# Optimization experiments

Measured on AMD Instinct MI355X. Metric: run time of the kernel, lower is better.

## Reference

```python
import jax, jax.numpy as jnp
import numpy as np

NUM_HEADS = 16
D_MODEL = 1024
DEPTH = D_MODEL // NUM_HEADS
THRESHOLD = 0.1
BATCH = 2
SEQ = 2048


def setup_inputs() -> dict:
    key = jax.random.key(0)
    ks = jax.random.split(key, 9)
    w_scale = 1.0 / np.sqrt(D_MODEL)
    Q = jax.random.normal(ks[0], (BATCH, SEQ, D_MODEL), dtype=jnp.float32)
    T = jax.random.normal(ks[1], (BATCH, SEQ, D_MODEL), dtype=jnp.float32)
    V = jax.random.normal(ks[2], (BATCH, SEQ, D_MODEL), dtype=jnp.float32)
    Wq = jax.random.normal(ks[3], (NUM_HEADS, D_MODEL, DEPTH), dtype=jnp.float32) * w_scale
    Wk = jax.random.normal(ks[4], (NUM_HEADS, D_MODEL, DEPTH), dtype=jnp.float32) * w_scale
    Wv = jax.random.normal(ks[5], (NUM_HEADS, D_MODEL, DEPTH), dtype=jnp.float32) * w_scale
    Wo = jax.random.normal(ks[6], (D_MODEL, D_MODEL), dtype=jnp.float32) * w_scale
    bq = jnp.zeros((NUM_HEADS, DEPTH), dtype=jnp.float32)
    bk = jnp.zeros((NUM_HEADS, DEPTH), dtype=jnp.float32)
    bv = jnp.zeros((NUM_HEADS, DEPTH), dtype=jnp.float32)
    bo = jnp.zeros((D_MODEL,), dtype=jnp.float32)
    return {"Q": Q, "T": T, "V": V, "Wq": Wq, "bq": bq, "Wk": Wk, "bk": bk,
            "Wv": Wv, "bv": bv, "Wo": Wo, "bo": bo}


def reference(Q, T, V, Wq, bq, Wk, bk, Wv, bv, Wo, bo):
    # Per-head projections (stacked over heads): [B,S,D] x [H,D,E] -> [B,H,S,E]
    q = jnp.einsum('bsd,hde->bhse', Q, Wq) + bq[None, :, None, :]
    k = jnp.einsum('bsd,hde->bhse', T, Wk) + bk[None, :, None, :]
    v = jnp.einsum('bsd,hde->bhse', V, Wv) + bv[None, :, None, :]

    # Raw scores (NOT pre-scaled): [B,H,S,S]
    scores = jnp.einsum('bhqe,bhke->bhqk', q, k)
    # tf.where(A>thr, A, -2**32 * cast(A>thr)) -> failing entries become 0
    scores = jnp.where(scores > THRESHOLD, scores, jnp.zeros((), scores.dtype))
    # M = 1 - lower_band(ones): +1 on strictly upper-triangular entries
    seq = scores.shape[-1]
    upper = jnp.triu(jnp.ones((seq, seq), dtype=scores.dtype), k=1)
    scores = (scores + upper) / jnp.sqrt(jnp.asarray(DEPTH, scores.dtype))

    attn = jax.nn.softmax(scores, axis=-1)
    out = jnp.einsum('bhqk,bhke->bhqe', attn, v)  # [B,H,S,E]
    B, H, S, E = out.shape
    concat = out.transpose(0, 2, 1, 3).reshape(B, S, H * E)  # [B,S,D]
    return concat @ Wo + bo
```

## Files before the change

### kernel.cpp

```cpp
#include <hip/hip_runtime.h>
#include <stdint.h>


typedef __attribute__((ext_vector_type(8))) short bf16x8;
typedef __attribute__((ext_vector_type(4))) float f32x4;

#define DEVFN static __device__ __forceinline__

static constexpr int S_ = 2048;
static constexpr int H_ = 16;

DEVFN unsigned short f2bf(float x) {
  union { float f; uint32_t u; } v; v.f = x;
  const uint32_t r = v.u + 0x7fffu + ((v.u >> 16) & 1u);
  return (unsigned short)(r >> 16);
}

DEVFN f32x4 fzero() { f32x4 v = {0.f, 0.f, 0.f, 0.f}; return v; }

union U8 { uint32_t u[4]; bf16x8 v; };

DEVFN void gld_lds16(const void* g, void* lds) {
  __builtin_amdgcn_global_load_lds(
      (const __attribute__((address_space(1))) void*)g,
      (__attribute__((address_space(3))) void*)lds, 16, 0, 0);
}

__global__ void prep_weights(const float* __restrict__ Wq, const float* __restrict__ Wk,
                             const float* __restrict__ Wv, const float* __restrict__ Wo,
                             unsigned short* __restrict__ dstBase) {
  const int z = blockIdx.z;
  const float* src = (z == 0) ? Wq : (z == 1) ? Wk : (z == 2) ? Wv : Wo;
  unsigned short* dst = dstBase + (size_t)z * (1024u * 1024u);
  const int idx = blockIdx.x * 256 + threadIdx.x;
  const int c = idx & 1023;
  const int d0 = (idx >> 10) << 3;
  unsigned short hv[8];
#pragma unroll
  for (int t = 0; t < 8; ++t) {
    const int d = d0 + t;
    const float v = (z < 3) ? src[(size_t)((c >> 6) * 1024 + d) * 64 + (c & 63)]
                            : src[(size_t)d * 1024 + c];
    hv[t] = f2bf(v);
  }
  *(uint4*)(dst + (size_t)c * 1024 + d0) = *(const uint4*)hv;
}

__global__ __launch_bounds__(256, 3)
void proj_gemm(const float* __restrict__ Qm, const float* __restrict__ Tm,
               const float* __restrict__ Vm, const unsigned short* __restrict__ Wt,
               const float* __restrict__ bq, const float* __restrict__ bk,
               const float* __restrict__ bv, unsigned short* __restrict__ qb,
               unsigned short* __restrict__ kb, unsigned short* __restrict__ vtb) {
  __shared__ float Af[2][128 * 32];
  __shared__ unsigned short Bt[2][128 * 32];

  const int tid = threadIdx.x;
  const int lane = tid & 63;
  const int w = tid >> 6;
  const int g = lane >> 4, c = lane & 15;
  const int wm = w >> 1, wn = w & 1;

  const int m0 = blockIdx.x * 128;
  const int proj = blockIdx.y >> 3;
  const int n0 = (blockIdx.y & 7) * 128;

  const float* Asrc = (proj == 0) ? Qm : (proj == 1) ? Tm : Vm;
  const unsigned short* W = Wt + (size_t)proj * (1024u * 1024u);

  f32x4 acc[4][4];
#pragma unroll
  for (int i = 0; i < 4; ++i)
#pragma unroll
    for (int j = 0; j < 4; ++j) acc[i][j] = fzero();

  const int arow = w * 8 + (lane >> 3);
  const int ach = lane & 7;
  const int brow = w * 16 + (lane >> 2);
  const int bch = lane & 3;

  auto stage = [&](int kt, int buf) {
#pragma unroll
    for (int u = 0; u < 4; ++u) {
      const int row = u * 32 + arow;
      const int ch = ach ^ (row & 7);
      gld_lds16(Asrc + (size_t)(m0 + row) * 1024 + kt * 32 + ch * 4,
                &Af[buf][(u * 32 + w * 8) * 32]);
    }
#pragma unroll
    for (int u = 0; u < 2; ++u) {
      const int row = u * 64 + brow;
      const int ch = bch ^ ((row >> 1) & 3);
      gld_lds16(W + (size_t)(n0 + row) * 1024 + kt * 32 + ch * 8,
                &Bt[buf][(u * 64 + w * 16) * 32]);
    }
  };

  stage(0, 0);
  __syncthreads();

  for (int kt = 0; kt < 32; ++kt) {
    const int buf = kt & 1;
    if (kt < 31) stage(kt + 1, buf ^ 1);

    bf16x8 af[4], bfr[4];
#pragma unroll
    for (int mi = 0; mi < 4; ++mi) {
      const int row = wm * 64 + mi * 16 + c;
      const int swz = row & 7;
      const float4 fa = *(const float4*)&Af[buf][row * 32 + ((2 * g) ^ swz) * 4];
      const float4 fb = *(const float4*)&Af[buf][row * 32 + ((2 * g + 1) ^ swz) * 4];
      U8 u8;
      asm("v_cvt_pk_bf16_f32 %0, %1, %2" : "=v"(u8.u[0]) : "v"(fa.x), "v"(fa.y));
      asm("v_cvt_pk_bf16_f32 %0, %1, %2" : "=v"(u8.u[1]) : "v"(fa.z), "v"(fa.w));
      asm("v_cvt_pk_bf16_f32 %0, %1, %2" : "=v"(u8.u[2]) : "v"(fb.x), "v"(fb.y));
      asm("v_cvt_pk_bf16_f32 %0, %1, %2" : "=v"(u8.u[3]) : "v"(fb.z), "v"(fb.w));
      af[mi] = u8.v;
    }
#pragma unroll
    for (int ni = 0; ni < 4; ++ni) {
      const int row = wn * 64 + ni * 16 + c;
      bfr[ni] = *(const bf16x8*)&Bt[buf][row * 32 + ((g ^ ((row >> 1) & 3))) * 8];
    }
#pragma unroll
    for (int mi = 0; mi < 4; ++mi)
#pragma unroll
      for (int ni = 0; ni < 4; ++ni)
        acc[mi][ni] = __builtin_amdgcn_mfma_f32_16x16x32_bf16(af[mi], bfr[ni],
                                                              acc[mi][ni], 0, 0, 0);
    __syncthreads();
  }

  const float* bias = (proj == 0) ? bq : (proj == 1) ? bk : bv;
  if (proj < 2) {
    unsigned short* dptr = (proj == 0) ? qb : kb;
#pragma unroll
    for (int ni = 0; ni < 4; ++ni) {
      const int colb = n0 + wn * 64 + ni * 16 + c;
      const float bc = bias[colb];
      const int hh = colb >> 6, e = colb & 63;
#pragma unroll
      for (int mi = 0; mi < 4; ++mi)
#pragma unroll
        for (int r = 0; r < 4; ++r) {
          const int row = m0 + wm * 64 + mi * 16 + g * 4 + r;
          const int bb = row >> 11, s = row & 2047;
          dptr[(((size_t)(bb * H_ + hh)) * S_ + s) * 64 + e] = f2bf(acc[mi][ni][r] + bc);
        }
    }
  } else {
#pragma unroll
    for (int ni = 0; ni < 4; ++ni) {
      const int colb = n0 + wn * 64 + ni * 16 + c;
      const float bc = bias[colb];
      const int hh = colb >> 6, e = colb & 63;
#pragma unroll
      for (int mi = 0; mi < 4; ++mi) {
        const int rowb = m0 + wm * 64 + mi * 16 + g * 4;
        const int bb = rowb >> 11, s0 = rowb & 2047;
        const float v0 = acc[mi][ni][0] + bc, v1 = acc[mi][ni][1] + bc;
        const float v2 = acc[mi][ni][2] + bc, v3 = acc[mi][ni][3] + bc;
        uint2 pk;
        asm("v_cvt_pk_bf16_f32 %0, %1, %2" : "=v"(pk.x) : "v"(v0), "v"(v1));
        asm("v_cvt_pk_bf16_f32 %0, %1, %2" : "=v"(pk.y) : "v"(v2), "v"(v3));
        *(uint2*)&vtb[(((size_t)(bb * H_ + hh)) * 64 + e) * S_ + s0] = pk;
      }
    }
  }
}

__global__ __launch_bounds__(256, 2)
void attn_kernel(const unsigned short* __restrict__ qb,
                 const unsigned short* __restrict__ kb,
                 const unsigned short* __restrict__ vtb,
                 unsigned short* __restrict__ att) {
  __shared__ unsigned short Kt[2][64 * 64];
  __shared__ unsigned short Vt[2][64 * 64];
  __shared__ unsigned short Pt[4][32 * 64];

  const int tid = threadIdx.x;
  const int lane = tid & 63;
  const int w = tid >> 6;
  const int g = lane >> 4, c = lane & 15;

  const int orig = blockIdx.x;
  const int logical = ((orig & 7) << 6) | (orig >> 3);
  const int qblk = logical & 15;
  const int bh = logical >> 4;
  const int hh = bh & 15, bz = bh >> 4;

  const int q0w = qblk * 128 + w * 32;
  const unsigned short* qh = qb + (size_t)bh * S_ * 64;
  const unsigned short* kh = kb + (size_t)bh * S_ * 64;
  const unsigned short* vh = vtb + (size_t)bh * 64 * S_;

  bf16x8 aq[2][2];
#pragma unroll
  for (int m = 0; m < 2; ++m)
#pragma unroll
    for (int t = 0; t < 2; ++t)
      aq[m][t] = *(const bf16x8*)&qh[(size_t)(q0w + m * 16 + c) * 64 + t * 32 + g * 8];

  bf16x8 onesB;
#pragma unroll
  for (int i = 0; i < 8; ++i) onesB[i] = (short)0x3F80;

  f32x4 O[2][4];
  f32x4 accL[2];
#pragma unroll
  for (int m = 0; m < 2; ++m) {
#pragma unroll
    for (int ne = 0; ne < 4; ++ne) O[m][ne] = fzero();
    accL[m] = fzero();
  }

  constexpr float L2E = 1.4426950408889634f;
  const float S2 = 0.125f * L2E;
  const float B2 = 0.125f * L2E;

  int kvOff[2][4], paOff[2][2], pwOff[2][4];
#pragma unroll
  for (int ks = 0; ks < 2; ++ks) {
#pragma unroll
    for (int mi = 0; mi < 4; ++mi) {
      const int row = mi * 16 + c;
      kvOff[ks][mi] = 2 * (row * 64 + ((ks * 4 + g) ^ (row & 7)) * 8);
    }
#pragma unroll
    for (int m = 0; m < 2; ++m)
      paOff[m][ks] = 2 * ((m * 16 + c) * 64 + ((ks * 4 + g) ^ (c & 7)) * 8);
  }
#pragma unroll
  for (int m = 0; m < 2; ++m)
#pragma unroll
    for (int mi = 0; mi < 4; ++mi)
      pwOff[m][mi] =
          2 * ((m * 16 + c) * 64 + ((2 * mi + (g >> 1)) ^ (c & 7)) * 8 + (g & 1) * 4);

  const int srow = w * 8 + (lane >> 3);
  const int sch = (lane & 7) ^ (srow & 7);
  const unsigned short* kS0 = kh + (size_t)srow * 64 + sch * 8;
  const unsigned short* kS1 = kh + (size_t)(32 + srow) * 64 + sch * 8;
  const unsigned short* vS0 = vh + (size_t)srow * S_ + sch * 8;
  const unsigned short* vS1 = vh + (size_t)(32 + srow) * S_ + sch * 8;

  {
    gld_lds16(kS0, &Kt[0][(w * 8) * 64]);
    gld_lds16(kS1, &Kt[0][(32 + w * 8) * 64]);
    gld_lds16(vS0, &Vt[0][(w * 8) * 64]);
    gld_lds16(vS1, &Vt[0][(32 + w * 8) * 64]);
  }
  __syncthreads();

#define SM_ELEM(M, MI)                                                         \
  do {                                                                         \
    float pv[4];                                                               \
    if (allUp || noneUp) {                                                     \
      const float bb = allUp ? B2 : 0.f;                                       \
      _Pragma("unroll")                                                        \
      for (int r = 0; r < 4; ++r) {                                            \
        const float v = sa[M][MI][r];                                          \
        pv[r] = __builtin_amdgcn_exp2f(                                        \
            (v > 0.1f) ? __builtin_fmaf(v, S2, bb) : bb);                      \
      }                                                                        \
    } else {                                                                   \
      const int iq = q0w + (M)*16 + c;                                         \
      _Pragma("unroll")                                                        \
      for (int r = 0; r < 4; ++r) {                                            \
        const float v = sa[M][MI][r];                                          \
        const float bb = (j0 + (MI)*16 + g * 4 + r > iq) ? B2 : 0.f;           \
        pv[r] = __builtin_amdgcn_exp2f(                                        \
            (v > 0.1f) ? __builtin_fmaf(v, S2, bb) : bb);                      \
      }                                                                        \
    }                                                                          \
    uint2 d;                                                                   \
    asm("v_cvt_pk_bf16_f32 %0, %1, %2" : "=v"(d.x) : "v"(pv[0]), "v"(pv[1])); \
    asm("v_cvt_pk_bf16_f32 %0, %1, %2" : "=v"(d.y) : "v"(pv[2]), "v"(pv[3])); \
    *(uint2*)((char*)&Pt[w][0] + pwOff[M][MI]) = d;                            \
  } while (0)

#define PV_HALF(KS, CUR)                                                       \
  do {                                                                         \
    const bf16x8 pa0 =                                                         \
        *(const bf16x8*)((const char*)&Pt[w][0] + paOff[0][KS]);               \
    const bf16x8 pa1 =                                                         \
        *(const bf16x8*)((const char*)&Pt[w][0] + paOff[1][KS]);               \
    accL[0] = __builtin_amdgcn_mfma_f32_16x16x32_bf16(pa0, onesB, accL[0],     \
                                                      0, 0, 0);                \
    accL[1] = __builtin_amdgcn_mfma_f32_16x16x32_bf16(pa1, onesB, accL[1],     \
                                                      0, 0, 0);                \
    _Pragma("unroll")                                                          \
    for (int ne = 0; ne < 4; ++ne) {                                           \
      const bf16x8 bv8 =                                                       \
          *(const bf16x8*)((const char*)&Vt[CUR][0] + kvOff[KS][ne]);          \
      O[0][ne] = __builtin_amdgcn_mfma_f32_16x16x32_bf16(pa0, bv8, O[0][ne],   \
                                                         0, 0, 0);             \
      O[1][ne] = __builtin_amdgcn_mfma_f32_16x16x32_bf16(pa1, bv8, O[1][ne],   \
                                                         0, 0, 0);             \
    }                                                                          \
  } while (0)

#define ATTN_BODY(JT, CUR)                                                     \
  do {                                                                         \
    const int j0 = (JT) * 64;                                                  \
    if ((JT) < 31) {             \
      gld_lds16(kS0 + 4096, &Kt[CUR ^ 1][(w * 8) * 64]);                       \
      gld_lds16(kS1 + 4096, &Kt[CUR ^ 1][(32 + w * 8) * 64]);                  \
      gld_lds16(vS0 + 64, &Vt[CUR ^ 1][(w * 8) * 64]);                         \
      gld_lds16(vS1 + 64, &Vt[CUR ^ 1][(32 + w * 8) * 64]);                    \
      kS0 += 4096; kS1 += 4096; vS0 += 64; vS1 += 64;                          \
    }                                                                          \
    f32x4 sa[2][4];                                                            \
    _Pragma("unroll")                                                          \
    for (int m = 0; m < 2; ++m)                                                \
      _Pragma("unroll")                                                        \
      for (int mi = 0; mi < 4; ++mi) sa[m][mi] = fzero();                      \
    __builtin_amdgcn_s_setprio(1);                                             \
    _Pragma("unroll")                                                          \
    for (int ks = 0; ks < 2; ++ks)                                             \
      _Pragma("unroll")                                                        \
      for (int mi = 0; mi < 4; ++mi) {                                         \
        const bf16x8 ka =                                                      \
            *(const bf16x8*)((const char*)&Kt[CUR][0] + kvOff[ks][mi]);        \
        sa[0][mi] = __builtin_amdgcn_mfma_f32_16x16x32_bf16(ka, aq[0][ks],     \
                                                            sa[0][mi], 0, 0, 0);\
        sa[1][mi] = __builtin_amdgcn_mfma_f32_16x16x32_bf16(ka, aq[1][ks],     \
                                                            sa[1][mi], 0, 0, 0);\
      }                                                                        \
    __builtin_amdgcn_s_setprio(0);                                             \
    const bool allUp = (j0 >= q0w + 32);                                       \
    const bool noneUp = (j0 + 63 <= q0w);                                      \
              \
    SM_ELEM(0, 0); SM_ELEM(0, 1); SM_ELEM(1, 0); SM_ELEM(1, 1);                \
    asm volatile("s_waitcnt lgkmcnt(0)" ::: "memory");                         \
    __builtin_amdgcn_sched_barrier(0);                                         \
    __builtin_amdgcn_s_setprio(1);                                             \
    PV_HALF(0, CUR);             \
    __builtin_amdgcn_s_setprio(0);                                             \
                                           \
    SM_ELEM(0, 2); SM_ELEM(0, 3); SM_ELEM(1, 2); SM_ELEM(1, 3);                \
    asm volatile("s_waitcnt lgkmcnt(0)" ::: "memory");                         \
    __builtin_amdgcn_sched_barrier(0);                                         \
    __builtin_amdgcn_s_setprio(1);                                             \
    PV_HALF(1, CUR);                                                           \
    __builtin_amdgcn_s_setprio(0);                                             \
    __syncthreads();     \
  } while (0)

  for (int jt = 0; jt < 32; jt += 2) {
    ATTN_BODY(jt, 0);
    ATTN_BODY(jt + 1, 1);
  }
#undef ATTN_BODY
#undef PV_HALF
#undef SM_ELEM

#pragma unroll
  for (int m = 0; m < 2; ++m)
#pragma unroll
    for (int r = 0; r < 4; ++r) {
      const float il = 1.f / accL[m][r];
      const int qg = q0w + m * 16 + g * 4 + r;
      const size_t ro = ((size_t)(bz * S_ + qg)) * 1024 + hh * 64;
#pragma unroll
      for (int ne = 0; ne < 4; ++ne)
        att[ro + ne * 16 + c] = f2bf(O[m][ne][r] * il);
    }
}

__global__ __launch_bounds__(256, 3)
void out_gemm(const unsigned short* __restrict__ att,
              const unsigned short* __restrict__ WoT,
              const float* __restrict__ bo, float* __restrict__ outp) {
  __shared__ unsigned short At[2][128 * 32];
  __shared__ unsigned short Bt[2][128 * 32];

  const int tid = threadIdx.x;
  const int lane = tid & 63;
  const int w = tid >> 6;
  const int g = lane >> 4, c = lane & 15;
  const int wm = w >> 1, wn = w & 1;
  const int m0 = blockIdx.x * 128;
  const int n0 = blockIdx.y * 128;

  f32x4 acc[4][4];
#pragma unroll
  for (int i = 0; i < 4; ++i)
#pragma unroll
    for (int j = 0; j < 4; ++j) acc[i][j] = fzero();

  const int srow = lane >> 2;
  const int sch = lane & 3;

  auto stage = [&](int kt, int buf) {
#pragma unroll
    for (int u = 0; u < 2; ++u) {
      const int row = u * 64 + w * 16 + srow;
      const int ch = sch ^ ((row >> 1) & 3);
      gld_lds16(att + (size_t)(m0 + row) * 1024 + kt * 32 + ch * 8,
                &At[buf][(u * 64 + w * 16) * 32]);
      gld_lds16(WoT + (size_t)(n0 + row) * 1024 + kt * 32 + ch * 8,
                &Bt[buf][(u * 64 + w * 16) * 32]);
    }
  };

  stage(0, 0);
  __syncthreads();

  for (int kt = 0; kt < 32; ++kt) {
    const int buf = kt & 1;
    if (kt < 31) stage(kt + 1, buf ^ 1);

    bf16x8 af[4], bfr[4];
#pragma unroll
    for (int mi = 0; mi < 4; ++mi) {
      const int row = wm * 64 + mi * 16 + c;
      af[mi] = *(const bf16x8*)&At[buf][row * 32 + ((g ^ ((row >> 1) & 3))) * 8];
    }
#pragma unroll
    for (int ni = 0; ni < 4; ++ni) {
      const int row = wn * 64 + ni * 16 + c;
      bfr[ni] = *(const bf16x8*)&Bt[buf][row * 32 + ((g ^ ((row >> 1) & 3))) * 8];
    }
#pragma unroll
    for (int mi = 0; mi < 4; ++mi)
#pragma unroll
      for (int ni = 0; ni < 4; ++ni)
        acc[mi][ni] = __builtin_amdgcn_mfma_f32_16x16x32_bf16(af[mi], bfr[ni],
                                                              acc[mi][ni], 0, 0, 0);
    __syncthreads();
  }

#pragma unroll
  for (int ni = 0; ni < 4; ++ni) {
    const int colb = n0 + wn * 64 + ni * 16 + c;
    const float bc = bo[colb];
#pragma unroll
    for (int mi = 0; mi < 4; ++mi)
#pragma unroll
      for (int r = 0; r < 4; ++r) {
        const int row = m0 + wm * 64 + mi * 16 + g * 4 + r;
        outp[(size_t)row * 1024 + colb] = acc[mi][ni][r] + bc;
      }
  }
}

extern "C" void kernel_launch(void* const* d_in, const int* in_sizes, int n_in,
                              void* d_out, int out_size, void* d_ws, size_t ws_size,
                              hipStream_t stream) {
  const float* Q  = (const float*)d_in[0];
  const float* T  = (const float*)d_in[1];
  const float* V  = (const float*)d_in[2];
  const float* Wq = (const float*)d_in[3];
  const float* bq = (const float*)d_in[4];
  const float* Wk = (const float*)d_in[5];
  const float* bk = (const float*)d_in[6];
  const float* Wv = (const float*)d_in[7];
  const float* bv = (const float*)d_in[8];
  const float* Wo = (const float*)d_in[9];
  const float* bo = (const float*)d_in[10];

  const size_t MB = 1024ull * 1024ull;
  if (ws_size < 40 * MB) return;

  uint8_t* ws = (uint8_t*)d_ws;
  unsigned short* Wt  = (unsigned short*)(ws);
  unsigned short* qb  = (unsigned short*)(ws + 8 * MB);
  unsigned short* kb  = (unsigned short*)(ws + 16 * MB);
  unsigned short* vtb = (unsigned short*)(ws + 24 * MB);
  unsigned short* attb = (unsigned short*)(ws + 32 * MB);

  prep_weights<<<dim3(512, 1, 4), 256, 0, stream>>>(Wq, Wk, Wv, Wo, Wt);
  proj_gemm<<<dim3(32, 24), 256, 0, stream>>>(Q, T, V, Wt, bq, bk, bv,
                                              qb, kb, vtb);
  attn_kernel<<<dim3(512), 256, 0, stream>>>(qb, kb, vtb, attb);
  out_gemm<<<dim3(32, 8), 256, 0, stream>>>(attb, Wt + 3ull * 1024ull * 1024ull,
                                            bo, (float*)d_out);
}
```

Before: 134.5 us.

## Load K and V fragments directly from global memory instead of LDS staging

Removes the double-buffered LDS staging of K and V tiles, along with their async global-to-LDS loads and per-tile block barriers. Each wave now reads its K and V MFMA fragments straight from global memory into registers every iteration. This cuts LDS traffic and synchronisation, but each of the four waves redundantly fetches the same K/V tile through the cache, and there is no explicit prefetch to hide global load latency. It also raises register pressure under the two-blocks-per-SM launch bound.

Result: slower. 193.2 us (+43.6%).

```diff
diff --git a/kernel.cpp b/kernel.cpp
--- a/kernel.cpp
+++ b/kernel.cpp
@@ -174,8 +174,6 @@
                  const unsigned short* __restrict__ kb,
                  const unsigned short* __restrict__ vtb,
                  unsigned short* __restrict__ att) {
-  __shared__ unsigned short Kt[2][64 * 64];
-  __shared__ unsigned short Vt[2][64 * 64];
   __shared__ unsigned short Pt[4][32 * 64];
 
   const int tid = threadIdx.x;
@@ -218,18 +216,12 @@
   const float S2 = 0.125f * L2E;
   const float B2 = 0.125f * L2E;
 
-  int kvOff[2][4], paOff[2][2], pwOff[2][4];
-#pragma unroll
-  for (int ks = 0; ks < 2; ++ks) {
-#pragma unroll
-    for (int mi = 0; mi < 4; ++mi) {
-      const int row = mi * 16 + c;
-      kvOff[ks][mi] = 2 * (row * 64 + ((ks * 4 + g) ^ (row & 7)) * 8);
-    }
+  int paOff[2][2], pwOff[2][4];
+#pragma unroll
+  for (int ks = 0; ks < 2; ++ks)
 #pragma unroll
     for (int m = 0; m < 2; ++m)
       paOff[m][ks] = 2 * ((m * 16 + c) * 64 + ((ks * 4 + g) ^ (c & 7)) * 8);
-  }
 #pragma unroll
   for (int m = 0; m < 2; ++m)
 #pragma unroll
@@ -237,20 +229,8 @@
       pwOff[m][mi] =
           2 * ((m * 16 + c) * 64 + ((2 * mi + (g >> 1)) ^ (c & 7)) * 8 + (g & 1) * 4);
 
-  const int srow = w * 8 + (lane >> 3);
-  const int sch = (lane & 7) ^ (srow & 7);
-  const unsigned short* kS0 = kh + (size_t)srow * 64 + sch * 8;
-  const unsigned short* kS1 = kh + (size_t)(32 + srow) * 64 + sch * 8;
-  const unsigned short* vS0 = vh + (size_t)srow * S_ + sch * 8;
-  const unsigned short* vS1 = vh + (size_t)(32 + srow) * S_ + sch * 8;
-
-  {
-    gld_lds16(kS0, &Kt[0][(w * 8) * 64]);
-    gld_lds16(kS1, &Kt[0][(32 + w * 8) * 64]);
-    gld_lds16(vS0, &Vt[0][(w * 8) * 64]);
-    gld_lds16(vS1, &Vt[0][(32 + w * 8) * 64]);
-  }
-  __syncthreads();
+  const unsigned short* kf = kh + (size_t)c * 64 + g * 8;
+  const unsigned short* vf = vh + (size_t)c * 2048 + g * 8;
 
 #define SM_ELEM(M, MI)                                                         \
   do {                                                                         \
@@ -279,80 +259,66 @@
     *(uint2*)((char*)&Pt[w][0] + pwOff[M][MI]) = d;                            \
   } while (0)
 
-#define PV_HALF(KS, CUR)                                                       \
-  do {                                                                         \
-    const bf16x8 pa0 =                                                         \
-        *(const bf16x8*)((const char*)&Pt[w][0] + paOff[0][KS]);               \
-    const bf16x8 pa1 =                                                         \
-        *(const bf16x8*)((const char*)&Pt[w][0] + paOff[1][KS]);               \
-    accL[0] = __builtin_amdgcn_mfma_f32_16x16x32_bf16(pa0, onesB, accL[0],     \
-                                                      0, 0, 0);                \
-    accL[1] = __builtin_amdgcn_mfma_f32_16x16x32_bf16(pa1, onesB, accL[1],     \
-                                                      0, 0, 0);                \
-    _Pragma("unroll")                                                          \
-    for (int ne = 0; ne < 4; ++ne) {                                           \
-      const bf16x8 bv8 =                                                       \
-          *(const bf16x8*)((const char*)&Vt[CUR][0] + kvOff[KS][ne]);          \
-      O[0][ne] = __builtin_amdgcn_mfma_f32_16x16x32_bf16(pa0, bv8, O[0][ne],   \
-                                                         0, 0, 0);             \
-      O[1][ne] = __builtin_amdgcn_mfma_f32_16x16x32_bf16(pa1, bv8, O[1][ne],   \
-                                                         0, 0, 0);             \
-    }                                                                          \
-  } while (0)
-
-#define ATTN_BODY(JT, CUR)                                                     \
-  do {                                                                         \
-    const int j0 = (JT) * 64;                                                  \
-    if ((JT) < 31) {             \
-      gld_lds16(kS0 + 4096, &Kt[CUR ^ 1][(w * 8) * 64]);                       \
-      gld_lds16(kS1 + 4096, &Kt[CUR ^ 1][(32 + w * 8) * 64]);                  \
-      gld_lds16(vS0 + 64, &Vt[CUR ^ 1][(w * 8) * 64]);                         \
-      gld_lds16(vS1 + 64, &Vt[CUR ^ 1][(32 + w * 8) * 64]);                    \
-      kS0 += 4096; kS1 += 4096; vS0 += 64; vS1 += 64;                          \
-    }                                                                          \
-    f32x4 sa[2][4];                                                            \
-    _Pragma("unroll")                                                          \
-    for (int m = 0; m < 2; ++m)                                                \
-      _Pragma("unroll")                                                        \
-      for (int mi = 0; mi < 4; ++mi) sa[m][mi] = fzero();                      \
-    __builtin_amdgcn_s_setprio(1);                                             \
-    _Pragma("unroll")                                                          \
-    for (int ks = 0; ks < 2; ++ks)                                             \
-      _Pragma("unroll")                                                        \
-      for (int mi = 0; mi < 4; ++mi) {                                         \
-        const bf16x8 ka =                                                      \
-            *(const bf16x8*)((const char*)&Kt[CUR][0] + kvOff[ks][mi]);        \
-        sa[0][mi] = __builtin_amdgcn_mfma_f32_16x16x32_bf16(ka, aq[0][ks],     \
-                                                            sa[0][mi], 0, 0, 0);\
-        sa[1][mi] = __builtin_amdgcn_mfma_f32_16x16x32_bf16(ka, aq[1][ks],     \
-                                                            sa[1][mi], 0, 0, 0);\
-      }                                                                        \
-    __builtin_amdgcn_s_setprio(0);                                             \
-    const bool allUp = (j0 >= q0w + 32);                                       \
-    const bool noneUp = (j0 + 63 <= q0w);                                      \
-              \
-    SM_ELEM(0, 0); SM_ELEM(0, 1); SM_ELEM(1, 0); SM_ELEM(1, 1);                \
-    asm volatile("s_waitcnt lgkmcnt(0)" ::: "memory");                         \
-    __builtin_amdgcn_sched_barrier(0);                                         \
-    __builtin_amdgcn_s_setprio(1);                                             \
-    PV_HALF(0, CUR);             \
-    __builtin_amdgcn_s_setprio(0);                                             \
-                                           \
-    SM_ELEM(0, 2); SM_ELEM(0, 3); SM_ELEM(1, 2); SM_ELEM(1, 3);                \
-    asm volatile("s_waitcnt lgkmcnt(0)" ::: "memory");                         \
-    __builtin_amdgcn_sched_barrier(0);                                         \
-    __builtin_amdgcn_s_setprio(1);                                             \
-    PV_HALF(1, CUR);                                                           \
-    __builtin_amdgcn_s_setprio(0);                                             \
-    __syncthreads();     \
-  } while (0)
-
-  for (int jt = 0; jt < 32; jt += 2) {
-    ATTN_BODY(jt, 0);
-    ATTN_BODY(jt + 1, 1);
-  }
-#undef ATTN_BODY
-#undef PV_HALF
+  for (int jt = 0; jt < 32; ++jt) {
+    const int j0 = jt * 64;
+    const unsigned short* kj = kf + (size_t)j0 * 64;
+    const unsigned short* vj = vf + j0;
+
+    bf16x8 ka[2][4], bv[2][4];
+#pragma unroll
+    for (int ks = 0; ks < 2; ++ks)
+#pragma unroll
+      for (int mi = 0; mi < 4; ++mi)
+        ka[ks][mi] = *(const bf16x8*)(kj + mi * 1024 + ks * 32);
+#pragma unroll
+    for (int ks = 0; ks < 2; ++ks)
+#pragma unroll
+      for (int ne = 0; ne < 4; ++ne)
+        bv[ks][ne] = *(const bf16x8*)(vj + (size_t)ne * 32768 + ks * 32);
+
+    f32x4 sa[2][4];
+#pragma unroll
+    for (int m = 0; m < 2; ++m)
+#pragma unroll
+      for (int mi = 0; mi < 4; ++mi) sa[m][mi] = fzero();
+    __builtin_amdgcn_s_setprio(1);
+#pragma unroll
+    for (int ks = 0; ks < 2; ++ks)
+#pragma unroll
+      for (int mi = 0; mi < 4; ++mi) {
+        sa[0][mi] = __builtin_amdgcn_mfma_f32_16x16x32_bf16(ka[ks][mi], aq[0][ks],
+                                                            sa[0][mi], 0, 0, 0);
+        sa[1][mi] = __builtin_amdgcn_mfma_f32_16x16x32_bf16(ka[ks][mi], aq[1][ks],
+                                                            sa[1][mi], 0, 0, 0);
+      }
+    __builtin_amdgcn_s_setprio(0);
+
+    const bool allUp = (j0 >= q0w + 32);
+    const bool noneUp = (j0 + 63 <= q0w);
+    SM_ELEM(0, 0); SM_ELEM(0, 1); SM_ELEM(0, 2); SM_ELEM(0, 3);
+    SM_ELEM(1, 0); SM_ELEM(1, 1); SM_ELEM(1, 2); SM_ELEM(1, 3);
+    asm volatile("s_waitcnt lgkmcnt(0)" ::: "memory");
+    __builtin_amdgcn_sched_barrier(0);
+
+    __builtin_amdgcn_s_setprio(1);
+#pragma unroll
+    for (int ks = 0; ks < 2; ++ks) {
+      const bf16x8 pa0 = *(const bf16x8*)((const char*)&Pt[w][0] + paOff[0][ks]);
+      const bf16x8 pa1 = *(const bf16x8*)((const char*)&Pt[w][0] + paOff[1][ks]);
+      accL[0] = __builtin_amdgcn_mfma_f32_16x16x32_bf16(pa0, onesB, accL[0],
+                                                        0, 0, 0);
+      accL[1] = __builtin_amdgcn_mfma_f32_16x16x32_bf16(pa1, onesB, accL[1],
+                                                        0, 0, 0);
+#pragma unroll
+      for (int ne = 0; ne < 4; ++ne) {
+        O[0][ne] = __builtin_amdgcn_mfma_f32_16x16x32_bf16(pa0, bv[ks][ne],
+                                                           O[0][ne], 0, 0, 0);
+        O[1][ne] = __builtin_amdgcn_mfma_f32_16x16x32_bf16(pa1, bv[ks][ne],
+                                                           O[1][ne], 0, 0, 0);
+      }
+    }
+    __builtin_amdgcn_s_setprio(0);
+  }
 #undef SM_ELEM
 
 #pragma unroll
```
